# Performance work log

Hardware: AMD Instinct MI355X
Metric: run time of the kernel (lower is better)

## Reference

```python
import jax, jax.numpy as jnp
import numpy as np

N, E, CIN, COUT = 50000, 800000, 61, 64
EPS = 1e-5


def batchnorm(h, g, b):
    # BatchNorm1d in training mode: batch stats (biased variance), affine
    m = jnp.mean(h, axis=0)
    v = jnp.var(h, axis=0)
    return g * (h - m) * jax.lax.rsqrt(v + EPS) + b


def setup_inputs() -> dict:
    key = jax.random.key(0)
    ks = jax.random.split(key, 7)
    x = jax.random.normal(ks[0], (N, CIN), jnp.float32)
    pos = jax.random.normal(ks[1], (N, 3), jnp.float32)
    edge_index = jax.random.randint(ks[2], (2, E), 0, N, dtype=jnp.int64)
    s1 = 1.0 / np.sqrt(CIN + 3)
    s2 = 1.0 / np.sqrt(COUT)
    ss = 1.0 / np.sqrt(CIN)
    W1 = jax.random.normal(ks[3], (CIN + 3, COUT), jnp.float32) * s1
    b1 = jnp.zeros((COUT,), jnp.float32)
    W2 = jax.random.normal(ks[4], (COUT, COUT), jnp.float32) * s2
    b2 = jnp.zeros((COUT,), jnp.float32)
    Ws = jax.random.normal(ks[5], (CIN, COUT), jnp.float32) * ss
    bs = jnp.zeros((COUT,), jnp.float32)
    ones = jnp.ones((COUT,), jnp.float32)
    zeros = jnp.zeros((COUT,), jnp.float32)
    return {
        "x": x, "pos": pos, "edge_index": edge_index,
        "W1": W1, "b1": b1, "g1": ones, "be1": zeros,
        "W2": W2, "b2": b2, "g2": ones, "be2": zeros,
        "Ws": Ws, "bs": bs, "gs": ones, "bes": zeros,
        "gf": ones, "bef": zeros,
    }


def reference(x, pos, edge_index, W1, b1, g1, be1, W2, b2, g2, be2,
              Ws, bs, gs, bes, gf, bef):
    src, dst = edge_index[0], edge_index[1]  # j -> i (source_to_target)
    # per-edge message: [x_j, pos_j - pos_i]  -> [E, CIN+3]
    msg = jnp.concatenate([x[src], pos[src] - pos[dst]], axis=-1)
    # local_nn = MLP([CIN+3, COUT, COUT]) with per-layer Lin -> ReLU -> BN
    h = batchnorm(jax.nn.relu(msg @ W1 + b1), g1, be1)
    h = batchnorm(jax.nn.relu(h @ W2 + b2), g2, be2)
    # scatter-max aggregation to destination nodes
    agg = jax.ops.segment_max(h, dst, num_segments=N)
    agg = jnp.where(jnp.isneginf(agg), 0.0, agg)  # nodes with no incoming edges
    # residual shortcut (Linear + BN since CIN != COUT)
    identity = batchnorm(x @ Ws + bs, gs, bes)
    return jax.nn.relu(batchnorm(agg, gf, bef) + identity)
```

## Files before the change

kernel.cpp:

```cpp
#include <hip/hip_runtime.h>

#define CIN 61
constexpr float EPS = 1e-5f;
constexpr double SCALE = 16777216.0;

using s16x8 = __attribute__((ext_vector_type(8))) short;
using fx4   = __attribute__((ext_vector_type(4))) float;

static __device__ __forceinline__ unsigned short f2bf(float f) {
  unsigned int u = __float_as_uint(f);
  u = (u + 0x7fffu + ((u >> 16) & 1u)) >> 16;
  return (unsigned short)u;
}
static __device__ __forceinline__ float bf2f(unsigned short h) {
  return __uint_as_float(((unsigned int)h) << 16);
}

__device__ __forceinline__ void stat_reduce(float val, float* red, long long* dst_ll) {
  int tid = threadIdx.x;
  red[tid] = val;
  __syncthreads();
  if (tid < 64) {
    float t = red[tid] + red[tid + 64] + red[tid + 128] + red[tid + 192];
    atomicAdd((unsigned long long*)&dst_ll[tid],
              (unsigned long long)(long long)((double)t * SCALE));
  }
  __syncthreads();
}

__global__ __launch_bounds__(256) void k_node(
    const float* __restrict__ x, const float* __restrict__ W1,
    const float* __restrict__ b1, const float* __restrict__ Ws,
    const float* __restrict__ bs, unsigned short* __restrict__ y,
    unsigned short* __restrict__ s_out, long long* __restrict__ stats, int N,
    const int* __restrict__ ei, unsigned int* __restrict__ hist,
    unsigned short* __restrict__ rank, int E) {
  const int tid = threadIdx.x, lane = tid & 63, wv = tid >> 6;
  float w1r[64], wsr[64];
#pragma unroll
  for (int k = 0; k < 64; ++k) {
    w1r[k] = (k < CIN) ? W1[k * 64 + lane] : 0.f;
    wsr[k] = (k < CIN) ? Ws[k * 64 + lane] : 0.f;
  }
  const float b1v = b1[lane], bsv = bs[lane];
  __shared__ float lrow[4][64];
  __shared__ float red[256];
  float ssum = 0.f, ssq = 0.f;
  const int nq = N >> 2;
  for (int q = blockIdx.x; q < nq; q += gridDim.x) {
    const int n = (q << 2) + wv;
    lrow[wv][lane] = (lane < CIN) ? x[(size_t)n * CIN + lane] : 0.f;
    __builtin_amdgcn_wave_barrier();
    float a0 = b1v, a1 = 0.f, a2 = 0.f, a3 = 0.f;
    float c0 = bsv, c1 = 0.f, c2 = 0.f, c3 = 0.f;
    const float4* rr = (const float4*)&lrow[wv][0];
#pragma unroll
    for (int k4 = 0; k4 < 16; ++k4) {
      float4 v = rr[k4];
      a0 = fmaf(v.x, w1r[4 * k4 + 0], a0);
      a1 = fmaf(v.y, w1r[4 * k4 + 1], a1);
      a2 = fmaf(v.z, w1r[4 * k4 + 2], a2);
      a3 = fmaf(v.w, w1r[4 * k4 + 3], a3);
      c0 = fmaf(v.x, wsr[4 * k4 + 0], c0);
      c1 = fmaf(v.y, wsr[4 * k4 + 1], c1);
      c2 = fmaf(v.z, wsr[4 * k4 + 2], c2);
      c3 = fmaf(v.w, wsr[4 * k4 + 3], c3);
    }
    y[(size_t)n * 64 + lane] = f2bf((a0 + a1) + (a2 + a3));
    const float sacc = (c0 + c1) + (c2 + c3);
    s_out[(size_t)n * 64 + lane] = f2bf(sacc);
    ssum += sacc;
    ssq = fmaf(sacc, sacc, ssq);
    __builtin_amdgcn_wave_barrier();
  }
  stat_reduce(ssum, red, stats + 256);
  stat_reduce(ssq, red, stats + 320);
  for (int i = blockIdx.x * 256 + tid; i < E; i += gridDim.x * 256) {
    const int dst = ei[E + i];
    rank[i] = (unsigned short)atomicAdd(&hist[dst], 1u);
  }
}

__global__ __launch_bounds__(256) void k_scan1(
    const unsigned int* __restrict__ hist, unsigned int* __restrict__ bsum) {
  const int tid = threadIdx.x, lane = tid & 63, wv = tid >> 6;
  const uint4 v = ((const uint4*)(hist + blockIdx.x * 1024))[tid];
  unsigned int s = v.x + v.y + v.z + v.w;
#pragma unroll
  for (int off = 1; off < 64; off <<= 1) s += __shfl_xor(s, off);
  __shared__ unsigned int wsum[4];
  if (lane == 0) wsum[wv] = s;
  __syncthreads();
  if (tid == 0) bsum[blockIdx.x] = wsum[0] + wsum[1] + wsum[2] + wsum[3];
}

__global__ __launch_bounds__(256) void k_scan3(
    const unsigned int* __restrict__ hist, const unsigned int* __restrict__ bsum,
    unsigned int* __restrict__ cursor0, unsigned short* __restrict__ dstS, int N) {
  const int tid = threadIdx.x, lane = tid & 63, wv = tid >> 6;
  __shared__ unsigned int s_boff;
  if (tid < 64) {
    unsigned int v = (tid < blockIdx.x) ? bsum[tid] : 0u;
#pragma unroll
    for (int off = 1; off < 64; off <<= 1) v += __shfl_xor(v, off);
    if (tid == 0) s_boff = v;
  }
  const uint4 v = ((const uint4*)(hist + blockIdx.x * 1024))[tid];
  const unsigned int s = v.x + v.y + v.z + v.w;
  unsigned int incl = s;
#pragma unroll
  for (int off = 1; off < 64; off <<= 1) {
    unsigned int u = __shfl_up(incl, off);
    if (lane >= off) incl += u;
  }
  __shared__ unsigned int wtot[4];
  if (lane == 63) wtot[wv] = incl;
  __syncthreads();
  unsigned int wb = s_boff;
#pragma unroll
  for (int k = 0; k < 4; ++k) wb += (k < wv) ? wtot[k] : 0u;
  const unsigned int ex = wb + incl - s;
  uint4 o;
  o.x = ex; o.y = ex + v.x; o.z = o.y + v.y; o.w = o.z + v.z;
  ((uint4*)(cursor0 + blockIdx.x * 1024))[tid] = o;
  const unsigned int d0 = blockIdx.x * 1024 + tid * 4;
  const unsigned int e4 = o.w + v.w;
  for (unsigned int i = o.x; i < o.y; ++i) dstS[i] = (unsigned short)d0;
  for (unsigned int i = o.y; i < o.z; ++i) dstS[i] = (unsigned short)(d0 + 1);
  for (unsigned int i = o.z; i < o.w; ++i) dstS[i] = (unsigned short)(d0 + 2);
  for (unsigned int i = o.w; i < e4;  ++i) dstS[i] = (unsigned short)(d0 + 3);
}

__global__ __launch_bounds__(256) void k_edge1(
    const int* __restrict__ ei, const float* __restrict__ pos,
    const unsigned short* __restrict__ y, const float* __restrict__ W1,
    const unsigned int* __restrict__ cursor0, const unsigned short* __restrict__ rank,
    unsigned short* __restrict__ t1S, long long* __restrict__ stats, int E) {
  const int tid = threadIdx.x, lane = tid & 63, wv = tid >> 6;
  const int g8 = lane >> 3, c8 = lane & 7;
  float wp[3][8];
#pragma unroll
  for (int d = 0; d < 3; ++d)
#pragma unroll
    for (int i = 0; i < 8; ++i) wp[d][i] = W1[(61 + d) * 64 + 8 * c8 + i];
  float ssum[8] = {0.f, 0.f, 0.f, 0.f, 0.f, 0.f, 0.f, 0.f};
  float ssq[8]  = {0.f, 0.f, 0.f, 0.f, 0.f, 0.f, 0.f, 0.f};
  const int ngrp = E >> 3;
  const int nw = gridDim.x * 4;
  for (int q = blockIdx.x * 4 + wv; q < ngrp; q += 4 * nw) {
    const int qB = q + nw, qC = q + 2 * nw, qD = q + 3 * nw;
    const bool hB = qB < ngrp, hC = qC < ngrp, hD = qD < ngrp;
    const int eA = (q << 3) + g8;
    const int eB = hB ? (qB << 3) + g8 : eA;
    const int eC = hC ? (qC << 3) + g8 : eA;
    const int eD = hD ? (qD << 3) + g8 : eA;
    const int srcA = ei[eA], dstA = ei[E + eA];
    const int srcB = ei[eB], dstB = ei[E + eB];
    const int srcC = ei[eC], dstC = ei[E + eC];
    const int srcD = ei[eD], dstD = ei[E + eD];
    float pvA = 0.f, pvB = 0.f, pvC = 0.f, pvD = 0.f;
    if (c8 < 3) {
      pvA = pos[srcA * 3 + c8] - pos[dstA * 3 + c8];
      pvB = pos[srcB * 3 + c8] - pos[dstB * 3 + c8];
      pvC = pos[srcC * 3 + c8] - pos[dstC * 3 + c8];
      pvD = pos[srcD * 3 + c8] - pos[dstD * 3 + c8];
    }
    const s16x8 yA = *(const s16x8*)(y + (unsigned)srcA * 64u + 8u * (unsigned)c8);
    const s16x8 yB = *(const s16x8*)(y + (unsigned)srcB * 64u + 8u * (unsigned)c8);
    const s16x8 yC = *(const s16x8*)(y + (unsigned)srcC * 64u + 8u * (unsigned)c8);
    const s16x8 yD = *(const s16x8*)(y + (unsigned)srcD * 64u + 8u * (unsigned)c8);
    unsigned offA = 0, offB = 0, offC = 0, offD = 0;
    if (c8 == 0) {
      offA = cursor0[dstA] + rank[eA];
      offB = cursor0[dstB] + rank[eB];
      offC = cursor0[dstC] + rank[eC];
      offD = cursor0[dstD] + rank[eD];
    }
#define EDGE1_BODY(PV, YV, OFFV)                                                \
    {                                                                           \
      const float p0 = __shfl(PV, g8 * 8 + 0);                                  \
      const float p1 = __shfl(PV, g8 * 8 + 1);                                  \
      const float p2 = __shfl(PV, g8 * 8 + 2);                                  \
      const unsigned off = __shfl(OFFV, g8 * 8 + 0);                            \
      union { s16x8 v; unsigned short s[8]; } tb;                               \
      _Pragma("unroll")                                                         \
      for (int i = 0; i < 8; ++i) {                                             \
        float v = bf2f((unsigned short)YV[i]);                                  \
        v = fmaf(p0, wp[0][i], v);                                              \
        v = fmaf(p1, wp[1][i], v);                                              \
        v = fmaf(p2, wp[2][i], v);                                              \
        v = fmaxf(v, 0.f);                                                      \
        ssum[i] += v;                                                           \
        ssq[i] = fmaf(v, v, ssq[i]);                                            \
        tb.s[i] = f2bf(v);                                                      \
      }                                                                         \
      *(s16x8*)(t1S + (size_t)off * 64 + 8 * c8) = tb.v;                        \
    }
    EDGE1_BODY(pvA, yA, offA)
    if (hB) EDGE1_BODY(pvB, yB, offB)
    if (hC) EDGE1_BODY(pvC, yC, offC)
    if (hD) EDGE1_BODY(pvD, yD, offD)
#undef EDGE1_BODY
  }
#pragma unroll
  for (int i = 0; i < 8; ++i) {
    ssum[i] += __shfl_xor(ssum[i], 8);
    ssum[i] += __shfl_xor(ssum[i], 16);
    ssum[i] += __shfl_xor(ssum[i], 32);
    ssq[i] += __shfl_xor(ssq[i], 8);
    ssq[i] += __shfl_xor(ssq[i], 16);
    ssq[i] += __shfl_xor(ssq[i], 32);
  }
  __shared__ float sred[2][64];
  if (tid < 128) ((float*)sred)[tid] = 0.f;
  __syncthreads();
  if (g8 == 0) {
#pragma unroll
    for (int i = 0; i < 8; ++i) {
      atomicAdd(&sred[0][8 * c8 + i], ssum[i]);
      atomicAdd(&sred[1][8 * c8 + i], ssq[i]);
    }
  }
  __syncthreads();
  if (tid < 64) {
    atomicAdd((unsigned long long*)&stats[0 + tid],
              (unsigned long long)(long long)((double)sred[0][tid] * SCALE));
    atomicAdd((unsigned long long*)&stats[64 + tid],
              (unsigned long long)(long long)((double)sred[1][tid] * SCALE));
  }
}

__global__ void k_coefA(const long long* __restrict__ stats,
                        const float* __restrict__ g1, const float* __restrict__ be1,
                        const float* __restrict__ W2, const float* __restrict__ b2,
                        unsigned short* __restrict__ bFpack,
                        float* __restrict__ biasF, double invE) {
  const int c = threadIdx.x;
  __shared__ float a1s[64], c1s[64], b2sh[64];
  double m = (double)stats[c] * invE;
  double v = (double)stats[64 + c] * invE - m * m;
  float a = g1[c] * rsqrtf((float)v + EPS);
  a1s[c] = a;
  c1s[c] = fmaf(-(float)m, a, be1[c]);
  __syncthreads();
  float acc = b2[c];
  for (int k = 0; k < 64; ++k) acc = fmaf(c1s[k], W2[k * 64 + c], acc);
  b2sh[c] = acc;
  const int lg = c >> 4, l15 = c & 15;
#pragma unroll
  for (int t = 0; t < 4; ++t)
#pragma unroll
    for (int s = 0; s < 2; ++s)
#pragma unroll
      for (int i = 0; i < 8; ++i) {
        const int k = s * 32 + lg * 8 + i;
        bFpack[c * 64 + t * 16 + s * 8 + i] = f2bf(a1s[k] * W2[k * 64 + l15 + 16 * t]);
      }
  __syncthreads();
  float4 bf;
  bf.x = b2sh[l15]; bf.y = b2sh[l15 + 16]; bf.z = b2sh[l15 + 32]; bf.w = b2sh[l15 + 48];
  ((float4*)biasF)[c] = bf;
}

__global__ __launch_bounds__(256) void k_edge2(
    const unsigned short* __restrict__ t1S, const unsigned short* __restrict__ dstS,
    const unsigned short* __restrict__ bFpack, const float* __restrict__ biasF,
    long long* __restrict__ stats, unsigned int* __restrict__ agg, int E) {
  const int tid = threadIdx.x, lane = tid & 63, wv = tid >> 6;
  const int l15 = lane & 15, lg = lane >> 4;
  s16x8 bF[4][2];
  {
    const s16x8* bfp = (const s16x8*)(bFpack + (size_t)lane * 64);
#pragma unroll
    for (int t = 0; t < 4; ++t)
#pragma unroll
      for (int s = 0; s < 2; ++s) bF[t][s] = bfp[t * 2 + s];
  }
  float bias[4];
  {
    const float4 bv = ((const float4*)biasF)[lane];
    bias[0] = bv.x; bias[1] = bv.y; bias[2] = bv.z; bias[3] = bv.w;
  }
  float ssum[4] = {0.f, 0.f, 0.f, 0.f}, ssq[4] = {0.f, 0.f, 0.f, 0.f};
  const int ntile = E >> 4;
  const int nw = gridDim.x * 4;
  int tile = blockIdx.x * 4 + wv;
  if (tile < ntile) {
    const unsigned short* ar0 = t1S + (size_t)((tile << 4) + l15) * 64 + (unsigned)(lg * 8);
    s16x8 aF0 = *(const s16x8*)ar0;
    s16x8 aF1 = *(const s16x8*)(ar0 + 32);
    int dstv = (int)dstS[(tile << 4) + l15];
    for (;;) {
      const int tn = tile + nw;
      const bool hn = tn < ntile;
      s16x8 aF0n, aF1n;
      int dstvn = 0;
      if (hn) {
        const unsigned short* arn =
            t1S + (size_t)((tn << 4) + l15) * 64 + (unsigned)(lg * 8);
        aF0n = *(const s16x8*)arn;
        aF1n = *(const s16x8*)(arn + 32);
        dstvn = (int)dstS[(tn << 4) + l15];
      }
      fx4 acc[4];
#pragma unroll
      for (int t = 0; t < 4; ++t) {
        acc[t][0] = bias[t]; acc[t][1] = bias[t];
        acc[t][2] = bias[t]; acc[t][3] = bias[t];
      }
#pragma unroll
      for (int t = 0; t < 4; ++t) {
        acc[t] = __builtin_amdgcn_mfma_f32_16x16x32_bf16(aF0, bF[t][0], acc[t], 0, 0, 0);
        acc[t] = __builtin_amdgcn_mfma_f32_16x16x32_bf16(aF1, bF[t][1], acc[t], 0, 0, 0);
      }
      float tv[4][4];
#pragma unroll
      for (int t = 0; t < 4; ++t)
#pragma unroll
        for (int j = 0; j < 4; ++j) {
          const float v = fmaxf(acc[t][j], 0.f);
          tv[t][j] = v;
          ssum[t] += v;
          ssq[t] = fmaf(v, v, ssq[t]);
        }
      const int prev = __shfl(dstv, (l15 + 15) & 15);
      const bool isb = (l15 == 0) || (dstv != prev);
      unsigned long long bm = __ballot(isb) & 0xFFFFull;
      while (bm) {
        const int r0 = __ffsll((long long)bm) - 1;
        bm &= bm - 1;
        const int r1 = bm ? (__ffsll((long long)bm) - 1) : 16;
        const int d = __shfl(dstv, r0);
        float lm[4];
#pragma unroll
        for (int t = 0; t < 4; ++t) {
          float m0 = 0.f;
#pragma unroll
          for (int j = 0; j < 4; ++j) {
            const int row = lg * 4 + j;
            m0 = fmaxf(m0, (row >= r0 && row < r1) ? tv[t][j] : 0.f);
          }
          m0 = fmaxf(m0, __shfl_xor(m0, 16));
          m0 = fmaxf(m0, __shfl_xor(m0, 32));
          lm[t] = m0;
        }
        const float val = (lg == 0) ? lm[0] : (lg == 1) ? lm[1] : (lg == 2) ? lm[2] : lm[3];
        atomicMax(&agg[(unsigned)d * 64u + (unsigned)(l15 + 16 * lg)],
                  __float_as_uint(val) | 0x80000000u);
      }
      if (!hn) break;
      tile = tn; aF0 = aF0n; aF1 = aF1n; dstv = dstvn;
    }
  }
#pragma unroll
  for (int t = 0; t < 4; ++t) {
    ssum[t] += __shfl_xor(ssum[t], 16); ssum[t] += __shfl_xor(ssum[t], 32);
    ssq[t]  += __shfl_xor(ssq[t], 16);  ssq[t]  += __shfl_xor(ssq[t], 32);
  }
  __shared__ float sred[2][64];
  if (tid < 128) ((float*)sred)[tid] = 0.f;
  __syncthreads();
  if (lg == 0) {
#pragma unroll
    for (int t = 0; t < 4; ++t) {
      atomicAdd(&sred[0][l15 + 16 * t], ssum[t]);
      atomicAdd(&sred[1][l15 + 16 * t], ssq[t]);
    }
  }
  __syncthreads();
  if (tid < 64) {
    atomicAdd((unsigned long long*)&stats[128 + tid],
              (unsigned long long)(long long)((double)sred[0][tid] * SCALE));
    atomicAdd((unsigned long long*)&stats[192 + tid],
              (unsigned long long)(long long)((double)sred[1][tid] * SCALE));
  }
}

__global__ __launch_bounds__(256) void k_aggfix(
    const unsigned int* __restrict__ agg, long long* __restrict__ stats, int total) {
  const int tid = threadIdx.x;
  __shared__ float red[256];
  float ssum = 0.f, ssq = 0.f, kcf = 0.f;
  const int step = gridDim.x * 256;
  for (int i = blockIdx.x * 256 + tid; i < total; i += step) {
    const unsigned int u = agg[i];
    if (u >> 31) {
      const float v = __uint_as_float(u & 0x7fffffffu);
      ssum += v;
      ssq = fmaf(v, v, ssq);
      if ((i & 63) == 0) kcf += 1.f;
    }
  }
  stat_reduce(ssum, red, stats + 384);
  stat_reduce(ssq, red, stats + 448);
  stat_reduce(kcf, red, stats + 512);
}

__global__ void k_coefB(const long long* __restrict__ stats,
                        const float* __restrict__ g2, const float* __restrict__ be2,
                        const float* __restrict__ gs, const float* __restrict__ bes,
                        const float* __restrict__ gf, const float* __restrict__ bef,
                        float* __restrict__ coef, double invE, double invN, int N) {
  const int c = threadIdx.x;
  double m2 = (double)stats[128 + c] * invE;
  double v2 = (double)stats[192 + c] * invE - m2 * m2;
  float a2 = g2[c] * rsqrtf((float)v2 + EPS);
  float c2 = fmaf(-(float)m2, a2, be2[c]);
  double mS = (double)stats[256 + c] * invN;
  double vS = (double)stats[320 + c] * invN - mS * mS;
  float aS = gs[c] * rsqrtf((float)vS + EPS);
  float cS = fmaf(-(float)mS, aS, bes[c]);
  double su = (double)stats[384 + c] / SCALE;
  double qu = (double)stats[448 + c] / SCALE;
  double K  = (double)stats[512] / SCALE;
  double sv = (double)a2 * su + (double)c2 * K;
  double qv = (double)a2 * a2 * qu + 2.0 * a2 * c2 * su + (double)c2 * c2 * K;
  double mv = sv / N;
  double vv = qv / N - mv * mv;
  float aF = gf[c] * rsqrtf((float)vv + EPS);
  float cF = fmaf(-(float)mv, aF, bef[c]);
  coef[c]       = aF * a2;
  coef[64 + c]  = fmaf(aF, c2, cF);
  coef[128 + c] = cF;
  coef[192 + c] = aS;
  coef[256 + c] = cS;
}

__global__ __launch_bounds__(256) void k_final(
    const unsigned int* __restrict__ agg, const unsigned short* __restrict__ sbuf,
    const float* __restrict__ coef, float* __restrict__ out, int total) {
  int i = blockIdx.x * 256 + threadIdx.x;
  if (i >= total) return;
  const int c = i & 63;
  const unsigned int u = agg[i];
  float base;
  if (u >> 31)
    base = fmaf(coef[c], __uint_as_float(u & 0x7fffffffu), coef[64 + c]);
  else
    base = coef[128 + c];
  const float sv = fmaf(coef[192 + c], bf2f(sbuf[i]), coef[256 + c]);
  out[i] = fmaxf(base + sv, 0.f);
}

extern "C" void kernel_launch(void* const* d_in, const int* in_sizes, int n_in,
                              void* d_out, int out_size, void* d_ws, size_t ws_size,
                              hipStream_t stream) {
  const float* x   = (const float*)d_in[0];
  const float* pos = (const float*)d_in[1];
  const int*   ei  = (const int*)d_in[2];
  const float* W1  = (const float*)d_in[3];
  const float* b1  = (const float*)d_in[4];
  const float* g1  = (const float*)d_in[5];
  const float* be1 = (const float*)d_in[6];
  const float* W2  = (const float*)d_in[7];
  const float* b2  = (const float*)d_in[8];
  const float* g2  = (const float*)d_in[9];
  const float* be2 = (const float*)d_in[10];
  const float* Ws  = (const float*)d_in[11];
  const float* bs  = (const float*)d_in[12];
  const float* gs  = (const float*)d_in[13];
  const float* bes = (const float*)d_in[14];
  const float* gf  = (const float*)d_in[15];
  const float* bef = (const float*)d_in[16];
  const int N = in_sizes[0] / CIN;
  const int E = in_sizes[2] / 2;

  char* ws = (char*)d_ws;
  const size_t o_stats = 0;
  const size_t o_bsum  = 4608;
  const size_t o_hist  = 8192;
  const size_t o_agg   = o_hist + 200704;
  const size_t zeroEnd = o_agg + (size_t)N * 256;
  const size_t o_curs0 = zeroEnd;
  const size_t o_coef  = o_curs0 + 200704;
  const size_t o_frag  = o_coef + 4096;
  const size_t o_rank  = o_frag + 12288;
  const size_t o_dstS  = o_rank + (size_t)E * 2;
  const size_t o_ybuf  = o_dstS + (size_t)E * 2;
  const size_t o_sbuf  = o_ybuf + (size_t)N * 128;
  const size_t o_t1S   = o_sbuf + (size_t)N * 128;

  long long* stats      = (long long*)(ws + o_stats);
  unsigned int* bsum    = (unsigned int*)(ws + o_bsum);
  unsigned int* hist    = (unsigned int*)(ws + o_hist);
  unsigned int* agg     = (unsigned int*)(ws + o_agg);
  unsigned int* cursor0 = (unsigned int*)(ws + o_curs0);
  float* coef           = (float*)(ws + o_coef);
  unsigned short* bFpack= (unsigned short*)(ws + o_frag);
  float* biasF          = (float*)(ws + o_frag + 8192);
  unsigned short* rank  = (unsigned short*)(ws + o_rank);
  unsigned short* dstS  = (unsigned short*)(ws + o_dstS);
  unsigned short* ybuf  = (unsigned short*)(ws + o_ybuf);
  unsigned short* sbuf  = (unsigned short*)(ws + o_sbuf);
  unsigned short* t1S   = (unsigned short*)(ws + o_t1S);

  const double invE = 1.0 / (SCALE * (double)E);
  const double invN = 1.0 / (SCALE * (double)N);
  const int total = N * 64;
  const int nScanBlk = 49;

  hipMemsetAsync(d_ws, 0, zeroEnd, stream);

  hipLaunchKernelGGL(k_node, dim3(1024), dim3(256), 0, stream,
                     x, W1, b1, Ws, bs, ybuf, sbuf, stats, N, ei, hist, rank, E);
  hipLaunchKernelGGL(k_scan1, dim3(nScanBlk), dim3(256), 0, stream, hist, bsum);
  hipLaunchKernelGGL(k_scan3, dim3(nScanBlk), dim3(256), 0, stream,
                     hist, bsum, cursor0, dstS, N);
  hipLaunchKernelGGL(k_edge1, dim3(2048), dim3(256), 0, stream,
                     ei, pos, ybuf, W1, cursor0, rank, t1S, stats, E);
  hipLaunchKernelGGL(k_coefA, dim3(1), dim3(64), 0, stream,
                     stats, g1, be1, W2, b2, bFpack, biasF, invE);
  hipLaunchKernelGGL(k_edge2, dim3(2048), dim3(256), 0, stream,
                     t1S, dstS, bFpack, biasF, stats, agg, E);
  hipLaunchKernelGGL(k_aggfix, dim3(1024), dim3(256), 0, stream, agg, stats, total);
  hipLaunchKernelGGL(k_coefB, dim3(1), dim3(64), 0, stream,
                     stats, g2, be2, gs, bes, gf, bef, coef, invE, invN, N);
  hipLaunchKernelGGL(k_final, dim3((total + 255) / 256), dim3(256), 0, stream,
                     agg, sbuf, coef, (float*)d_out, total);
}
```

Baseline: 264.0 us.

## Move node linear layers to bf16 MFMA and split rank histogram kernel

Replaces the scalar-FMA node kernel (per-lane weight registers, one row per wave) with an MFMA bf16 kernel that processes 16-row tiles, using weight fragments pre-packed by a new tiny pack kernel. The edge-rank histogram pass is moved into its own kernel, and the software prefetch in the edge2 loop is removed in favour of a simple loop. This cuts FP32 ALU work and register pressure in the node stage, at the cost of two extra launches and bf16 rounding of x before the matmul.

```diff
diff --git a/kernel.cpp b/kernel.cpp
--- a/kernel.cpp
+++ b/kernel.cpp
@@ -28,54 +28,135 @@
   __syncthreads();
 }
 
-__global__ __launch_bounds__(256) void k_node(
-    const float* __restrict__ x, const float* __restrict__ W1,
-    const float* __restrict__ b1, const float* __restrict__ Ws,
-    const float* __restrict__ bs, unsigned short* __restrict__ y,
-    unsigned short* __restrict__ s_out, long long* __restrict__ stats, int N,
+__global__ void k_pack(const float* __restrict__ W1, const float* __restrict__ b1,
+                       const float* __restrict__ Ws, const float* __restrict__ bs,
+                       unsigned short* __restrict__ w1pk, unsigned short* __restrict__ wspk,
+                       float* __restrict__ biasY, float* __restrict__ biasS) {
+  const int c = threadIdx.x;
+  const int lg = c >> 4, l15 = c & 15;
+#pragma unroll
+  for (int t = 0; t < 4; ++t)
+#pragma unroll
+    for (int s = 0; s < 2; ++s)
+#pragma unroll
+      for (int i = 0; i < 8; ++i) {
+        const int k = s * 32 + lg * 8 + i;
+        const int col = l15 + 16 * t;
+        const int idx = c * 64 + t * 16 + s * 8 + i;
+        w1pk[idx] = (k < CIN) ? f2bf(W1[k * 64 + col]) : 0;
+        wspk[idx] = (k < CIN) ? f2bf(Ws[k * 64 + col]) : 0;
+      }
+  float4 by, bv;
+  by.x = b1[l15]; by.y = b1[l15 + 16]; by.z = b1[l15 + 32]; by.w = b1[l15 + 48];
+  bv.x = bs[l15]; bv.y = bs[l15 + 16]; bv.z = bs[l15 + 32]; bv.w = bs[l15 + 48];
+  ((float4*)biasY)[c] = by;
+  ((float4*)biasS)[c] = bv;
+}
+
+__global__ __launch_bounds__(256) void k_nodeM(
+    const float* __restrict__ x, const unsigned short* __restrict__ w1pk,
+    const unsigned short* __restrict__ wspk, const float* __restrict__ biasY,
+    const float* __restrict__ biasS, unsigned short* __restrict__ y,
+    unsigned short* __restrict__ s_out, long long* __restrict__ stats, int N) {
+  const int tid = threadIdx.x, lane = tid & 63, wv = tid >> 6;
+  const int l15 = lane & 15, lg = lane >> 4;
+  s16x8 bFy[4][2], bFs[4][2];
+  {
+    const s16x8* py = (const s16x8*)(w1pk + (size_t)lane * 64);
+    const s16x8* ps = (const s16x8*)(wspk + (size_t)lane * 64);
+#pragma unroll
+    for (int t = 0; t < 4; ++t)
+#pragma unroll
+      for (int s = 0; s < 2; ++s) {
+        bFy[t][s] = py[t * 2 + s];
+        bFs[t][s] = ps[t * 2 + s];
+      }
+  }
+  const float4 by = ((const float4*)biasY)[lane];
+  const float4 bv = ((const float4*)biasS)[lane];
+  const float biasy[4] = {by.x, by.y, by.z, by.w};
+  const float biass[4] = {bv.x, bv.y, bv.z, bv.w};
+  float ssum[4] = {0.f, 0.f, 0.f, 0.f}, ssq[4] = {0.f, 0.f, 0.f, 0.f};
+  const int ntile = N >> 4;
+  const int nw = gridDim.x * 4;
+  for (int tile = blockIdx.x * 4 + wv; tile < ntile; tile += nw) {
+    const int row = (tile << 4) + l15;
+    const float* xr = x + (size_t)row * CIN + lg * 8;
+    float xa[8], xb[8];
+#pragma unroll
+    for (int i = 0; i < 8; ++i) xa[i] = xr[i];
+#pragma unroll
+    for (int i = 0; i < 4; ++i) xb[i] = xr[32 + i];
+    if (lg < 3) {
+#pragma unroll
+      for (int i = 4; i < 8; ++i) xb[i] = xr[32 + i];
+    } else {
+      xb[4] = xr[36];
+      xb[5] = 0.f; xb[6] = 0.f; xb[7] = 0.f;
+    }
+    union { s16x8 v; unsigned int u[4]; } a0, a1;
+#pragma unroll
+    for (int h = 0; h < 4; ++h) {
+      asm("v_cvt_pk_bf16_f32 %0, %1, %2" : "=v"(a0.u[h]) : "v"(xa[2 * h]), "v"(xa[2 * h + 1]));
+      asm("v_cvt_pk_bf16_f32 %0, %1, %2" : "=v"(a1.u[h]) : "v"(xb[2 * h]), "v"(xb[2 * h + 1]));
+    }
+    fx4 accY[4], accS[4];
+#pragma unroll
+    for (int t = 0; t < 4; ++t) {
+      accY[t][0] = biasy[t]; accY[t][1] = biasy[t];
+      accY[t][2] = biasy[t]; accY[t][3] = biasy[t];
+      accS[t][0] = biass[t]; accS[t][1] = biass[t];
+      accS[t][2] = biass[t]; accS[t][3] = biass[t];
+    }
+#pragma unroll
+    for (int t = 0; t < 4; ++t) {
+      accY[t] = __builtin_amdgcn_mfma_f32_16x16x32_bf16(a0.v, bFy[t][0], accY[t], 0, 0, 0);
+      accY[t] = __builtin_amdgcn_mfma_f32_16x16x32_bf16(a1.v, bFy[t][1], accY[t], 0, 0, 0);
+      accS[t] = __builtin_amdgcn_mfma_f32_16x16x32_bf16(a0.v, bFs[t][0], accS[t], 0, 0, 0);
+      accS[t] = __builtin_amdgcn_mfma_f32_16x16x32_bf16(a1.v, bFs[t][1], accS[t], 0, 0, 0);
+    }
+#pragma unroll
+    for (int t = 0; t < 4; ++t) {
+      const unsigned col = (unsigned)(l15 + 16 * t);
+#pragma unroll
+      for (int j = 0; j < 4; ++j) {
+        const size_t ro = (size_t)((tile << 4) + lg * 4 + j) * 64 + col;
+        y[ro] = f2bf(accY[t][j]);
+        const float sv = accS[t][j];
+        s_out[ro] = f2bf(sv);
+        ssum[t] += sv;
+        ssq[t] = fmaf(sv, sv, ssq[t]);
+      }
+    }
+  }
+#pragma unroll
+  for (int t = 0; t < 4; ++t) {
+    ssum[t] += __shfl_xor(ssum[t], 16); ssum[t] += __shfl_xor(ssum[t], 32);
+    ssq[t]  += __shfl_xor(ssq[t], 16);  ssq[t]  += __shfl_xor(ssq[t], 32);
+  }
+  __shared__ float sred[2][64];
+  if (tid < 128) ((float*)sred)[tid] = 0.f;
+  __syncthreads();
+  if (lg == 0) {
+#pragma unroll
+    for (int t = 0; t < 4; ++t) {
+      atomicAdd(&sred[0][l15 + 16 * t], ssum[t]);
+      atomicAdd(&sred[1][l15 + 16 * t], ssq[t]);
+    }
+  }
+  __syncthreads();
+  if (tid < 64) {
+    atomicAdd((unsigned long long*)&stats[256 + tid],
+              (unsigned long long)(long long)((double)sred[0][tid] * SCALE));
+    atomicAdd((unsigned long long*)&stats[320 + tid],
+              (unsigned long long)(long long)((double)sred[1][tid] * SCALE));
+  }
+}
+
+__global__ __launch_bounds__(256) void k_rank(
     const int* __restrict__ ei, unsigned int* __restrict__ hist,
     unsigned short* __restrict__ rank, int E) {
-  const int tid = threadIdx.x, lane = tid & 63, wv = tid >> 6;
-  float w1r[64], wsr[64];
-#pragma unroll
-  for (int k = 0; k < 64; ++k) {
-    w1r[k] = (k < CIN) ? W1[k * 64 + lane] : 0.f;
-    wsr[k] = (k < CIN) ? Ws[k * 64 + lane] : 0.f;
-  }
-  const float b1v = b1[lane], bsv = bs[lane];
-  __shared__ float lrow[4][64];
-  __shared__ float red[256];
-  float ssum = 0.f, ssq = 0.f;
-  const int nq = N >> 2;
-  for (int q = blockIdx.x; q < nq; q += gridDim.x) {
-    const int n = (q << 2) + wv;
-    lrow[wv][lane] = (lane < CIN) ? x[(size_t)n * CIN + lane] : 0.f;
-    __builtin_amdgcn_wave_barrier();
-    float a0 = b1v, a1 = 0.f, a2 = 0.f, a3 = 0.f;
-    float c0 = bsv, c1 = 0.f, c2 = 0.f, c3 = 0.f;
-    const float4* rr = (const float4*)&lrow[wv][0];
-#pragma unroll
-    for (int k4 = 0; k4 < 16; ++k4) {
-      float4 v = rr[k4];
-      a0 = fmaf(v.x, w1r[4 * k4 + 0], a0);
-      a1 = fmaf(v.y, w1r[4 * k4 + 1], a1);
-      a2 = fmaf(v.z, w1r[4 * k4 + 2], a2);
-      a3 = fmaf(v.w, w1r[4 * k4 + 3], a3);
-      c0 = fmaf(v.x, wsr[4 * k4 + 0], c0);
-      c1 = fmaf(v.y, wsr[4 * k4 + 1], c1);
-      c2 = fmaf(v.z, wsr[4 * k4 + 2], c2);
-      c3 = fmaf(v.w, wsr[4 * k4 + 3], c3);
-    }
-    y[(size_t)n * 64 + lane] = f2bf((a0 + a1) + (a2 + a3));
-    const float sacc = (c0 + c1) + (c2 + c3);
-    s_out[(size_t)n * 64 + lane] = f2bf(sacc);
-    ssum += sacc;
-    ssq = fmaf(sacc, sacc, ssq);
-    __builtin_amdgcn_wave_barrier();
-  }
-  stat_reduce(ssum, red, stats + 256);
-  stat_reduce(ssq, red, stats + 320);
-  for (int i = blockIdx.x * 256 + tid; i < E; i += gridDim.x * 256) {
+  for (int i = blockIdx.x * 256 + threadIdx.x; i < E; i += gridDim.x * 256) {
     const int dst = ei[E + i];
     rank[i] = (unsigned short)atomicAdd(&hist[dst], 1u);
   }
@@ -284,72 +365,57 @@
   float ssum[4] = {0.f, 0.f, 0.f, 0.f}, ssq[4] = {0.f, 0.f, 0.f, 0.f};
   const int ntile = E >> 4;
   const int nw = gridDim.x * 4;
-  int tile = blockIdx.x * 4 + wv;
-  if (tile < ntile) {
-    const unsigned short* ar0 = t1S + (size_t)((tile << 4) + l15) * 64 + (unsigned)(lg * 8);
-    s16x8 aF0 = *(const s16x8*)ar0;
-    s16x8 aF1 = *(const s16x8*)(ar0 + 32);
-    int dstv = (int)dstS[(tile << 4) + l15];
-    for (;;) {
-      const int tn = tile + nw;
-      const bool hn = tn < ntile;
-      s16x8 aF0n, aF1n;
-      int dstvn = 0;
-      if (hn) {
-        const unsigned short* arn =
-            t1S + (size_t)((tn << 4) + l15) * 64 + (unsigned)(lg * 8);
-        aF0n = *(const s16x8*)arn;
-        aF1n = *(const s16x8*)(arn + 32);
-        dstvn = (int)dstS[(tn << 4) + l15];
+  for (int tile = blockIdx.x * 4 + wv; tile < ntile; tile += nw) {
+    const int rbase = tile << 4;
+    const unsigned short* ar = t1S + (size_t)(rbase + l15) * 64 + (unsigned)(lg * 8);
+    const s16x8 aF0 = *(const s16x8*)ar;
+    const s16x8 aF1 = *(const s16x8*)(ar + 32);
+    const int dstv = (int)dstS[rbase + l15];
+    fx4 acc[4];
+#pragma unroll
+    for (int t = 0; t < 4; ++t) {
+      acc[t][0] = bias[t]; acc[t][1] = bias[t];
+      acc[t][2] = bias[t]; acc[t][3] = bias[t];
+    }
+#pragma unroll
+    for (int t = 0; t < 4; ++t) {
+      acc[t] = __builtin_amdgcn_mfma_f32_16x16x32_bf16(aF0, bF[t][0], acc[t], 0, 0, 0);
+      acc[t] = __builtin_amdgcn_mfma_f32_16x16x32_bf16(aF1, bF[t][1], acc[t], 0, 0, 0);
+    }
+    float tv[4][4];
+#pragma unroll
+    for (int t = 0; t < 4; ++t)
+#pragma unroll
+      for (int j = 0; j < 4; ++j) {
+        const float v = fmaxf(acc[t][j], 0.f);
+        tv[t][j] = v;
+        ssum[t] += v;
+        ssq[t] = fmaf(v, v, ssq[t]);
       }
-      fx4 acc[4];
+    const int prev = __shfl(dstv, (l15 + 15) & 15);
+    const bool isb = (l15 == 0) || (dstv != prev);
+    unsigned long long bm = __ballot(isb) & 0xFFFFull;
+    while (bm) {
+      const int r0 = __ffsll((long long)bm) - 1;
+      bm &= bm - 1;
+      const int r1 = bm ? (__ffsll((long long)bm) - 1) : 16;
+      const int d = __shfl(dstv, r0);
+      float lm[4];
 #pragma unroll
       for (int t = 0; t < 4; ++t) {
-        acc[t][0] = bias[t]; acc[t][1] = bias[t];
-        acc[t][2] = bias[t]; acc[t][3] = bias[t];
+        float m0 = 0.f;
+#pragma unroll
+        for (int j = 0; j < 4; ++j) {
+          const int row = lg * 4 + j;
+          m0 = fmaxf(m0, (row >= r0 && row < r1) ? tv[t][j] : 0.f);
+        }
+        m0 = fmaxf(m0, __shfl_xor(m0, 16));
+        m0 = fmaxf(m0, __shfl_xor(m0, 32));
+        lm[t] = m0;
       }
-#pragma unroll
-      for (int t = 0; t < 4; ++t) {
-        acc[t] = __builtin_amdgcn_mfma_f32_16x16x32_bf16(aF0, bF[t][0], acc[t], 0, 0, 0);
-        acc[t] = __builtin_amdgcn_mfma_f32_16x16x32_bf16(aF1, bF[t][1], acc[t], 0, 0, 0);
-      }
-      float tv[4][4];
-#pragma unroll
-      for (int t = 0; t < 4; ++t)
-#pragma unroll
-        for (int j = 0; j < 4; ++j) {
-          const float v = fmaxf(acc[t][j], 0.f);
-          tv[t][j] = v;
-          ssum[t] += v;
-          ssq[t] = fmaf(v, v, ssq[t]);
-        }
-      const int prev = __shfl(dstv, (l15 + 15) & 15);
-      const bool isb = (l15 == 0) || (dstv != prev);
-      unsigned long long bm = __ballot(isb) & 0xFFFFull;
-      while (bm) {
-        const int r0 = __ffsll((long long)bm) - 1;
-        bm &= bm - 1;
-        const int r1 = bm ? (__ffsll((long long)bm) - 1) : 16;
-        const int d = __shfl(dstv, r0);
-        float lm[4];
-#pragma unroll
-        for (int t = 0; t < 4; ++t) {
-          float m0 = 0.f;
-#pragma unroll
-          for (int j = 0; j < 4; ++j) {
-            const int row = lg * 4 + j;
-            m0 = fmaxf(m0, (row >= r0 && row < r1) ? tv[t][j] : 0.f);
-          }
-          m0 = fmaxf(m0, __shfl_xor(m0, 16));
-          m0 = fmaxf(m0, __shfl_xor(m0, 32));
-          lm[t] = m0;
-        }
-        const float val = (lg == 0) ? lm[0] : (lg == 1) ? lm[1] : (lg == 2) ? lm[2] : lm[3];
-        atomicMax(&agg[(unsigned)d * 64u + (unsigned)(l15 + 16 * lg)],
-                  __float_as_uint(val) | 0x80000000u);
-      }
-      if (!hn) break;
-      tile = tn; aF0 = aF0n; aF1 = aF1n; dstv = dstvn;
+      const float val = (lg == 0) ? lm[0] : (lg == 1) ? lm[1] : (lg == 2) ? lm[2] : lm[3];
+      atomicMax(&agg[(unsigned)d * 64u + (unsigned)(l15 + 16 * lg)],
+                __float_as_uint(val) | 0x80000000u);
     }
   }
 #pragma unroll
@@ -474,7 +540,8 @@
   const size_t o_curs0 = zeroEnd;
   const size_t o_coef  = o_curs0 + 200704;
   const size_t o_frag  = o_coef + 4096;
-  const size_t o_rank  = o_frag + 12288;
+  const size_t o_pack  = o_frag + 12288;
+  const size_t o_rank  = o_pack + 18432;
   const size_t o_dstS  = o_rank + (size_t)E * 2;
   const size_t o_ybuf  = o_dstS + (size_t)E * 2;
   const size_t o_sbuf  = o_ybuf + (size_t)N * 128;
@@ -488,6 +555,10 @@
   float* coef           = (float*)(ws + o_coef);
   unsigned short* bFpack= (unsigned short*)(ws + o_frag);
   float* biasF          = (float*)(ws + o_frag + 8192);
+  unsigned short* w1pk  = (unsigned short*)(ws + o_pack);
+  unsigned short* wspk  = (unsigned short*)(ws + o_pack + 8192);
+  float* biasY          = (float*)(ws + o_pack + 16384);
+  float* biasS          = (float*)(ws + o_pack + 17408);
   unsigned short* rank  = (unsigned short*)(ws + o_rank);
   unsigned short* dstS  = (unsigned short*)(ws + o_dstS);
   unsigned short* ybuf  = (unsigned short*)(ws + o_ybuf);
@@ -501,8 +572,11 @@
 
   hipMemsetAsync(d_ws, 0, zeroEnd, stream);
 
-  hipLaunchKernelGGL(k_node, dim3(1024), dim3(256), 0, stream,
-                     x, W1, b1, Ws, bs, ybuf, sbuf, stats, N, ei, hist, rank, E);
+  hipLaunchKernelGGL(k_pack, dim3(1), dim3(64), 0, stream,
+                     W1, b1, Ws, bs, w1pk, wspk, biasY, biasS);
+  hipLaunchKernelGGL(k_nodeM, dim3(782), dim3(256), 0, stream,
+                     x, w1pk, wspk, biasY, biasS, ybuf, sbuf, stats, N);
+  hipLaunchKernelGGL(k_rank, dim3(1024), dim3(256), 0, stream, ei, hist, rank, E);
   hipLaunchKernelGGL(k_scan1, dim3(nScanBlk), dim3(256), 0, stream, hist, bsum);
   hipLaunchKernelGGL(k_scan3, dim3(nScanBlk), dim3(256), 0, stream,
                      hist, bsum, cursor0, dstS, N);
```

Result: slower. 292.2 us (+10.7%).

## Replace edge-tile atomic max with per-destination segmented reduction in edge2

Applied to the files above, without the earlier changes.

k_edge2 now loops over destination nodes using the CSR cursor offsets. It computes each node's edges in 16-row MFMA tiles, reduces the max in registers and writes agg with a plain store instead of atomicMax. This removes the dstS array, its fill loop in scan3 and the memset of the agg buffer; aggfix and final now use hist to detect empty nodes. The cost is partial tiles wasted on low-degree nodes (average degree about 16, so padding rows are recomputed) and possible load imbalance across waves.

```diff
diff --git a/kernel.cpp b/kernel.cpp
--- a/kernel.cpp
+++ b/kernel.cpp
@@ -96,7 +96,7 @@
 
 __global__ __launch_bounds__(256) void k_scan3(
     const unsigned int* __restrict__ hist, const unsigned int* __restrict__ bsum,
-    unsigned int* __restrict__ cursor0, unsigned short* __restrict__ dstS, int N) {
+    unsigned int* __restrict__ cursor0) {
   const int tid = threadIdx.x, lane = tid & 63, wv = tid >> 6;
   __shared__ unsigned int s_boff;
   if (tid < 64) {
@@ -123,12 +123,6 @@
   uint4 o;
   o.x = ex; o.y = ex + v.x; o.z = o.y + v.y; o.w = o.z + v.z;
   ((uint4*)(cursor0 + blockIdx.x * 1024))[tid] = o;
-  const unsigned int d0 = blockIdx.x * 1024 + tid * 4;
-  const unsigned int e4 = o.w + v.w;
-  for (unsigned int i = o.x; i < o.y; ++i) dstS[i] = (unsigned short)d0;
-  for (unsigned int i = o.y; i < o.z; ++i) dstS[i] = (unsigned short)(d0 + 1);
-  for (unsigned int i = o.z; i < o.w; ++i) dstS[i] = (unsigned short)(d0 + 2);
-  for (unsigned int i = o.w; i < e4;  ++i) dstS[i] = (unsigned short)(d0 + 3);
 }
 
 __global__ __launch_bounds__(256) void k_edge1(
@@ -263,9 +257,9 @@
 }
 
 __global__ __launch_bounds__(256) void k_edge2(
-    const unsigned short* __restrict__ t1S, const unsigned short* __restrict__ dstS,
+    const unsigned short* __restrict__ t1S, const unsigned int* __restrict__ cursor0,
     const unsigned short* __restrict__ bFpack, const float* __restrict__ biasF,
-    long long* __restrict__ stats, unsigned int* __restrict__ agg, int E) {
+    long long* __restrict__ stats, float* __restrict__ agg, int N) {
   const int tid = threadIdx.x, lane = tid & 63, wv = tid >> 6;
   const int l15 = lane & 15, lg = lane >> 4;
   s16x8 bF[4][2];
@@ -282,26 +276,19 @@
     bias[0] = bv.x; bias[1] = bv.y; bias[2] = bv.z; bias[3] = bv.w;
   }
   float ssum[4] = {0.f, 0.f, 0.f, 0.f}, ssq[4] = {0.f, 0.f, 0.f, 0.f};
-  const int ntile = E >> 4;
   const int nw = gridDim.x * 4;
-  int tile = blockIdx.x * 4 + wv;
-  if (tile < ntile) {
-    const unsigned short* ar0 = t1S + (size_t)((tile << 4) + l15) * 64 + (unsigned)(lg * 8);
-    s16x8 aF0 = *(const s16x8*)ar0;
-    s16x8 aF1 = *(const s16x8*)(ar0 + 32);
-    int dstv = (int)dstS[(tile << 4) + l15];
-    for (;;) {
-      const int tn = tile + nw;
-      const bool hn = tn < ntile;
-      s16x8 aF0n, aF1n;
-      int dstvn = 0;
-      if (hn) {
-        const unsigned short* arn =
-            t1S + (size_t)((tn << 4) + l15) * 64 + (unsigned)(lg * 8);
-        aF0n = *(const s16x8*)arn;
-        aF1n = *(const s16x8*)(arn + 32);
-        dstvn = (int)dstS[(tn << 4) + l15];
-      }
+  for (int d = blockIdx.x * 4 + wv; d < N; d += nw) {
+    const unsigned lo = cursor0[d];
+    const unsigned deg = cursor0[d + 1] - lo;
+    if (deg == 0) continue;
+    const unsigned last = lo + deg - 1u;
+    float mx[4] = {0.f, 0.f, 0.f, 0.f};
+    for (unsigned base = 0; base < deg; base += 16u) {
+      unsigned gr = lo + base + (unsigned)l15;
+      if (gr > last) gr = last;
+      const unsigned short* ar = t1S + (size_t)gr * 64 + (unsigned)(lg * 8);
+      const s16x8 aF0 = *(const s16x8*)ar;
+      const s16x8 aF1 = *(const s16x8*)(ar + 32);
       fx4 acc[4];
 #pragma unroll
       for (int t = 0; t < 4; ++t) {
@@ -313,44 +300,27 @@
         acc[t] = __builtin_amdgcn_mfma_f32_16x16x32_bf16(aF0, bF[t][0], acc[t], 0, 0, 0);
         acc[t] = __builtin_amdgcn_mfma_f32_16x16x32_bf16(aF1, bF[t][1], acc[t], 0, 0, 0);
       }
-      float tv[4][4];
+      const int rem = (int)(deg - base);
 #pragma unroll
       for (int t = 0; t < 4; ++t)
 #pragma unroll
         for (int j = 0; j < 4; ++j) {
           const float v = fmaxf(acc[t][j], 0.f);
-          tv[t][j] = v;
-          ssum[t] += v;
-          ssq[t] = fmaf(v, v, ssq[t]);
+          mx[t] = fmaxf(mx[t], v);
+          const int row = lg * 4 + j;
+          if (row < rem) {
+            ssum[t] += v;
+            ssq[t] = fmaf(v, v, ssq[t]);
+          }
         }
-      const int prev = __shfl(dstv, (l15 + 15) & 15);
-      const bool isb = (l15 == 0) || (dstv != prev);
-      unsigned long long bm = __ballot(isb) & 0xFFFFull;
-      while (bm) {
-        const int r0 = __ffsll((long long)bm) - 1;
-        bm &= bm - 1;
-        const int r1 = bm ? (__ffsll((long long)bm) - 1) : 16;
-        const int d = __shfl(dstv, r0);
-        float lm[4];
-#pragma unroll
-        for (int t = 0; t < 4; ++t) {
-          float m0 = 0.f;
-#pragma unroll
-          for (int j = 0; j < 4; ++j) {
-            const int row = lg * 4 + j;
-            m0 = fmaxf(m0, (row >= r0 && row < r1) ? tv[t][j] : 0.f);
-          }
-          m0 = fmaxf(m0, __shfl_xor(m0, 16));
-          m0 = fmaxf(m0, __shfl_xor(m0, 32));
-          lm[t] = m0;
-        }
-        const float val = (lg == 0) ? lm[0] : (lg == 1) ? lm[1] : (lg == 2) ? lm[2] : lm[3];
-        atomicMax(&agg[(unsigned)d * 64u + (unsigned)(l15 + 16 * lg)],
-                  __float_as_uint(val) | 0x80000000u);
-      }
-      if (!hn) break;
-      tile = tn; aF0 = aF0n; aF1 = aF1n; dstv = dstvn;
-    }
+    }
+#pragma unroll
+    for (int t = 0; t < 4; ++t) {
+      mx[t] = fmaxf(mx[t], __shfl_xor(mx[t], 16));
+      mx[t] = fmaxf(mx[t], __shfl_xor(mx[t], 32));
+    }
+    const float val = (lg == 0) ? mx[0] : (lg == 1) ? mx[1] : (lg == 2) ? mx[2] : mx[3];
+    agg[(size_t)d * 64 + (unsigned)(l15 + 16 * lg)] = val;
   }
 #pragma unroll
   for (int t = 0; t < 4; ++t) {
@@ -377,15 +347,15 @@
 }
 
 __global__ __launch_bounds__(256) void k_aggfix(
-    const unsigned int* __restrict__ agg, long long* __restrict__ stats, int total) {
+    const float* __restrict__ agg, const unsigned int* __restrict__ hist,
+    long long* __restrict__ stats, int total) {
   const int tid = threadIdx.x;
   __shared__ float red[256];
   float ssum = 0.f, ssq = 0.f, kcf = 0.f;
   const int step = gridDim.x * 256;
   for (int i = blockIdx.x * 256 + tid; i < total; i += step) {
-    const unsigned int u = agg[i];
-    if (u >> 31) {
-      const float v = __uint_as_float(u & 0x7fffffffu);
+    if (hist[i >> 6]) {
+      const float v = agg[i];
       ssum += v;
       ssq = fmaf(v, v, ssq);
       if ((i & 63) == 0) kcf += 1.f;
@@ -427,15 +397,15 @@
 }
 
 __global__ __launch_bounds__(256) void k_final(
-    const unsigned int* __restrict__ agg, const unsigned short* __restrict__ sbuf,
-    const float* __restrict__ coef, float* __restrict__ out, int total) {
+    const float* __restrict__ agg, const unsigned int* __restrict__ hist,
+    const unsigned short* __restrict__ sbuf, const float* __restrict__ coef,
+    float* __restrict__ out, int total) {
   int i = blockIdx.x * 256 + threadIdx.x;
   if (i >= total) return;
   const int c = i & 63;
-  const unsigned int u = agg[i];
   float base;
-  if (u >> 31)
-    base = fmaf(coef[c], __uint_as_float(u & 0x7fffffffu), coef[64 + c]);
+  if (hist[i >> 6])
+    base = fmaf(coef[c], agg[i], coef[64 + c]);
   else
     base = coef[128 + c];
   const float sv = fmaf(coef[192 + c], bf2f(sbuf[i]), coef[256 + c]);
@@ -469,27 +439,25 @@
   const size_t o_stats = 0;
   const size_t o_bsum  = 4608;
   const size_t o_hist  = 8192;
-  const size_t o_agg   = o_hist + 200704;
-  const size_t zeroEnd = o_agg + (size_t)N * 256;
-  const size_t o_curs0 = zeroEnd;
+  const size_t zeroEnd = o_hist + 200704;
+  const size_t o_agg   = zeroEnd;
+  const size_t o_curs0 = o_agg + (size_t)N * 256;
   const size_t o_coef  = o_curs0 + 200704;
   const size_t o_frag  = o_coef + 4096;
   const size_t o_rank  = o_frag + 12288;
-  const size_t o_dstS  = o_rank + (size_t)E * 2;
-  const size_t o_ybuf  = o_dstS + (size_t)E * 2;
+  const size_t o_ybuf  = o_rank + (size_t)E * 2;
   const size_t o_sbuf  = o_ybuf + (size_t)N * 128;
   const size_t o_t1S   = o_sbuf + (size_t)N * 128;
 
   long long* stats      = (long long*)(ws + o_stats);
   unsigned int* bsum    = (unsigned int*)(ws + o_bsum);
   unsigned int* hist    = (unsigned int*)(ws + o_hist);
-  unsigned int* agg     = (unsigned int*)(ws + o_agg);
+  float* agg            = (float*)(ws + o_agg);
   unsigned int* cursor0 = (unsigned int*)(ws + o_curs0);
   float* coef           = (float*)(ws + o_coef);
   unsigned short* bFpack= (unsigned short*)(ws + o_frag);
   float* biasF          = (float*)(ws + o_frag + 8192);
   unsigned short* rank  = (unsigned short*)(ws + o_rank);
-  unsigned short* dstS  = (unsigned short*)(ws + o_dstS);
   unsigned short* ybuf  = (unsigned short*)(ws + o_ybuf);
   unsigned short* sbuf  = (unsigned short*)(ws + o_sbuf);
   unsigned short* t1S   = (unsigned short*)(ws + o_t1S);
@@ -505,16 +473,17 @@
                      x, W1, b1, Ws, bs, ybuf, sbuf, stats, N, ei, hist, rank, E);
   hipLaunchKernelGGL(k_scan1, dim3(nScanBlk), dim3(256), 0, stream, hist, bsum);
   hipLaunchKernelGGL(k_scan3, dim3(nScanBlk), dim3(256), 0, stream,
-                     hist, bsum, cursor0, dstS, N);
+                     hist, bsum, cursor0);
   hipLaunchKernelGGL(k_edge1, dim3(2048), dim3(256), 0, stream,
                      ei, pos, ybuf, W1, cursor0, rank, t1S, stats, E);
   hipLaunchKernelGGL(k_coefA, dim3(1), dim3(64), 0, stream,
                      stats, g1, be1, W2, b2, bFpack, biasF, invE);
   hipLaunchKernelGGL(k_edge2, dim3(2048), dim3(256), 0, stream,
-                     t1S, dstS, bFpack, biasF, stats, agg, E);
-  hipLaunchKernelGGL(k_aggfix, dim3(1024), dim3(256), 0, stream, agg, stats, total);
+                     t1S, cursor0, bFpack, biasF, stats, agg, N);
+  hipLaunchKernelGGL(k_aggfix, dim3(1024), dim3(256), 0, stream,
+                     agg, hist, stats, total);
   hipLaunchKernelGGL(k_coefB, dim3(1), dim3(64), 0, stream,
                      stats, g2, be2, gs, bes, gf, bef, coef, invE, invN, N);
   hipLaunchKernelGGL(k_final, dim3((total + 255) / 256), dim3(256), 0, stream,
-                     agg, sbuf, coef, (float*)d_out, total);
-}
+                     agg, hist, sbuf, coef, (float*)d_out, total);
+}
```

New measurement: 252.0 us. 4.5% less time.
